# Kernel tuning notes

Measured on AMD Instinct MI355X. Metric: run time of the kernel, lower is better.

Reference implementation:

```python
import jax, jax.numpy as jnp
import numpy as np

B, IN_DIM, OUT_DIM = 16384, 1024, 512
N_CAPS, CAP_DIM = 8, 16


def squash(x, axis=-1):
    # scale = |x|^2 / (1 + |x|^2) ; out = scale * x / sqrt(|x|^2 + 1e-8)
    sq = jnp.sum(x * x, axis=axis, keepdims=True)
    return (sq / (1.0 + sq)) * x / jnp.sqrt(sq + 1e-8)


def setup_inputs() -> dict:
    key = jax.random.key(0)
    k1, k2, k3, k4 = jax.random.split(key, 4)
    x = jax.random.normal(k1, (B, IN_DIM), dtype=jnp.float32)
    # Linear(in_dim, n_caps*cap_dim) params (kaiming-ish scale)
    Wp = jax.random.normal(k2, (IN_DIM, N_CAPS * CAP_DIM), dtype=jnp.float32) / np.sqrt(IN_DIM)
    bp = jax.random.normal(k3, (N_CAPS * CAP_DIM,), dtype=jnp.float32) * 0.01
    # routing transform W: [n_caps, cap_dim, out_dim], init std 0.02 as in torch code
    W = jax.random.normal(k4, (N_CAPS, CAP_DIM, OUT_DIM), dtype=jnp.float32) * 0.02
    return {"x": x, "Wp": Wp, "bp": bp, "W": W, "n_routing": 3}


def reference(x, Wp, bp, W, n_routing):
    batch = x.shape[0]
    primary = x @ Wp + bp                                   # [B, n*d]
    primary = primary.reshape(batch, N_CAPS, CAP_DIM)       # [B, n, d]
    primary = squash(primary, axis=-1)
    u_hat = jnp.einsum('bnd,ndo->bno', primary, W)          # [B, n, o]
    b = jnp.zeros((batch, N_CAPS, 1), dtype=x.dtype)
    v = None
    for i in range(n_routing):
        c = jax.nn.softmax(b, axis=1)                       # [B, n, 1]
        s = jnp.sum(c * u_hat, axis=1)                      # [B, o]
        v = squash(s, axis=-1)                              # [B, o]
        if i < n_routing - 1:
            agreement = jnp.einsum('bno,bo->bn', u_hat, v)  # [B, n]
            b = b + agreement[..., None]
    return v
```

## Files before the change

kernel.cpp:

```cpp
#include <hip/hip_runtime.h>
#include <math.h>

typedef __attribute__((ext_vector_type(8))) short bf16x8;
typedef __attribute__((ext_vector_type(8))) unsigned short u16x8;
typedef __attribute__((ext_vector_type(4))) float f32x4;

__device__ __forceinline__ unsigned short f2bf(float f) {
  unsigned u = __float_as_uint(f);
  return (unsigned short)((u + 0x7FFFu + ((u >> 16) & 1u)) >> 16);
}
__device__ __forceinline__ float bf2f(unsigned short h) {
  return __uint_as_float(((unsigned)h) << 16);
}
__device__ __forceinline__ void cvt8(const float4& a, const float4& b,
                                     u16x8& h, u16x8& l) {
  float f[8] = {a.x, a.y, a.z, a.w, b.x, b.y, b.z, b.w};
#pragma unroll
  for (int i = 0; i < 8; ++i) {
    unsigned short hh = f2bf(f[i]);
    h[i] = hh;
    l[i] = f2bf(f[i] - bf2f(hh));
  }
}

__device__ const int PM36[36] = {0,0,0,0,0,0,0,0, 1,1,1,1,1,1,1, 2,2,2,2,2,2,
                                 3,3,3,3,3, 4,4,4,4, 5,5,5, 6,6, 7};
__device__ const int PN36[36] = {0,1,2,3,4,5,6,7, 1,2,3,4,5,6,7, 2,3,4,5,6,7,
                                 3,4,5,6,7, 4,5,6,7, 5,6,7, 6,7, 7};
__device__ __forceinline__ constexpr int gidx(int a, int b) {
  int m = a < b ? a : b, n = a < b ? b : a;
  return m * 8 - (m * (m - 1)) / 2 + (n - m);
}

__global__ __launch_bounds__(256) void caps_prep(
    const float* __restrict__ Wp, unsigned short* __restrict__ th,
    unsigned short* __restrict__ tl)
{
  __shared__ float tile[64][128];
  const int t = threadIdx.x, b = blockIdx.x;
  const float* src = Wp + (size_t)b * 64 * 128;
#pragma unroll
  for (int i = 0; i < 8; ++i) {
    int j = t + i * 256;
    int kk = j >> 5, q = j & 31;
    *(float4*)&tile[kk][q * 4] = *(const float4*)(src + kk * 128 + q * 4);
  }
  __syncthreads();
  const int col = t >> 1, kg0 = (t & 1) * 4;
  unsigned short hi[32], lo[32];
#pragma unroll
  for (int kk = 0; kk < 32; ++kk) {
    float v = tile[kg0 * 8 + kk][col];
    unsigned short h = f2bf(v);
    hi[kk] = h;
    lo[kk] = f2bf(v - bf2f(h));
  }
#pragma unroll
  for (int i = 0; i < 4; ++i) {
    size_t off = (size_t)b * 8192 + (size_t)(kg0 + i) * 1024 + (size_t)col * 8;
    u16x8 vh, vl;
#pragma unroll
    for (int e = 0; e < 8; ++e) { vh[e] = hi[i * 8 + e]; vl[e] = lo[i * 8 + e]; }
    *(u16x8*)(th + off) = vh;
    *(u16x8*)(tl + off) = vl;
  }
}

__global__ __launch_bounds__(256) void caps_prep2(
    const float* __restrict__ W, unsigned short* __restrict__ th,
    unsigned short* __restrict__ tl)
{
  int t = blockIdx.x * 256 + threadIdx.x;
#pragma unroll
  for (int h = 0; h < 2; ++h) {
    int c = t + h * 4096;
    int kt = c >> 12, rem = c & 4095;
    int kg = rem >> 9, col = rem & 511;
    int kbase = kt * 64 + kg * 8;
    u16x8 vh, vl;
#pragma unroll
    for (int e = 0; e < 8; ++e) {
      float v = W[(size_t)(kbase + e) * 512 + col];
      unsigned short hh = f2bf(v);
      vh[e] = hh;
      vl[e] = f2bf(v - bf2f(hh));
    }
    size_t off = ((size_t)(kt * 8 + kg) * 512 + col) * 8;
    *(u16x8*)(th + off) = vh;
    *(u16x8*)(tl + off) = vl;
  }
}

__global__ __launch_bounds__(256) void caps_gram(
    const float* __restrict__ W, float* __restrict__ M)
{
  int a = blockIdx.x * 16 + (threadIdx.x >> 4);
  int b = blockIdx.y * 16 + (threadIdx.x & 15);
  const float* wa = W + (size_t)a * 512;
  const float* wb = W + (size_t)b * 512;
  float acc = 0.f;
#pragma unroll 4
  for (int o = 0; o < 512; o += 4) {
    float4 x = *(const float4*)(wa + o);
    float4 y = *(const float4*)(wb + o);
    acc += x.x * y.x + x.y * y.y + x.z * y.z + x.w * y.w;
  }
  M[a * 128 + b] = acc;
}

#define LDSBUF 24576

__global__ __launch_bounds__(512) void caps_primary(
    const float* __restrict__ x, const unsigned short* __restrict__ bth,
    const unsigned short* __restrict__ btl, const float* __restrict__ bp,
    float* __restrict__ p_out)
{
  __shared__ unsigned short lds[2 * LDSBUF];
  const int tid  = threadIdx.x;
  const int lane = tid & 63;
  const int w    = tid >> 6;
  const int wm   = w >> 1;
  const int wn   = w & 1;
  const int row0 = blockIdx.x * 64;

  const int rowA = tid & 63;
  const int kgA  = tid >> 6;
  const float* xrow = x + (size_t)(row0 + rowA) * 1024;

  f32x4 acc[4];
#pragma unroll
  for (int j = 0; j < 4; ++j) acc[j] = (f32x4){0.f, 0.f, 0.f, 0.f};

  float4 a0, a1;
  u16x8 b0, b1, b2, b3;

#define STAGE_LOAD(kt) do { \
    const float* xp = xrow + (kt) * 64; \
    a0 = *(const float4*)(xp + kgA * 8); \
    a1 = *(const float4*)(xp + kgA * 8 + 4); \
    const unsigned short* bh_ = bth + (size_t)(kt) * 8192; \
    const unsigned short* bl_ = btl + (size_t)(kt) * 8192; \
    b0 = *(const u16x8*)(bh_ + (size_t)tid * 8); \
    b1 = *(const u16x8*)(bh_ + (size_t)(512 + tid) * 8); \
    b2 = *(const u16x8*)(bl_ + (size_t)tid * 8); \
    b3 = *(const u16x8*)(bl_ + (size_t)(512 + tid) * 8); \
  } while (0)

#define STAGE_WRITE(bufi) do { \
    u16x8 h0, l0; \
    cvt8(a0, a1, h0, l0); \
    unsigned short* B = lds + (bufi) * LDSBUF; \
    *(u16x8*)(B + kgA * 512 + rowA * 8) = h0; \
    *(u16x8*)(B + 4096 + kgA * 512 + rowA * 8) = l0; \
    *(u16x8*)(B + 8192  + tid * 8) = b0; \
    *(u16x8*)(B + 8192  + (512 + tid) * 8) = b1; \
    *(u16x8*)(B + 16384 + tid * 8) = b2; \
    *(u16x8*)(B + 16384 + (512 + tid) * 8) = b3; \
  } while (0)

#define COMPUTE(bufi) do { \
    const unsigned short* B = lds + (bufi) * LDSBUF; \
    _Pragma("unroll") \
    for (int s = 0; s < 2; ++s) { \
      const int kg = s * 4 + (lane >> 4); \
      const int rA = wm * 16 + (lane & 15); \
      const int cB = wn * 64 + (lane & 15); \
      bf16x8 ah = *(const bf16x8*)(B + kg * 512 + rA * 8); \
      bf16x8 al = *(const bf16x8*)(B + 4096 + kg * 512 + rA * 8); \
      _Pragma("unroll") \
      for (int nf = 0; nf < 4; ++nf) { \
        bf16x8 bh  = *(const bf16x8*)(B + 8192  + kg * 1024 + (cB + nf * 16) * 8); \
        bf16x8 blo = *(const bf16x8*)(B + 16384 + kg * 1024 + (cB + nf * 16) * 8); \
        acc[nf] = __builtin_amdgcn_mfma_f32_16x16x32_bf16(ah, bh,  acc[nf], 0, 0, 0); \
        acc[nf] = __builtin_amdgcn_mfma_f32_16x16x32_bf16(ah, blo, acc[nf], 0, 0, 0); \
        acc[nf] = __builtin_amdgcn_mfma_f32_16x16x32_bf16(al, bh,  acc[nf], 0, 0, 0); \
      } \
    } \
  } while (0)

  STAGE_LOAD(0);
  STAGE_WRITE(0);
  __syncthreads();
  for (int kt = 0; kt < 16; ++kt) {
    const int cur = kt & 1;
    if (kt < 15) STAGE_LOAD(kt + 1);
    COMPUTE(cur);
    if (kt < 15) STAGE_WRITE(cur ^ 1);
    __syncthreads();
  }

  const int ln = lane & 15, l4 = lane >> 4;
  float bpv[4];
#pragma unroll
  for (int nf = 0; nf < 4; ++nf) bpv[nf] = bp[wn * 64 + nf * 16 + ln];
#pragma unroll
  for (int nf = 0; nf < 4; ++nf)
#pragma unroll
    for (int r = 0; r < 4; ++r) {
      float val = acc[nf][r] + bpv[nf];
      float sq = val * val;
      sq += __shfl_xor(sq, 1); sq += __shfl_xor(sq, 2);
      sq += __shfl_xor(sq, 4); sq += __shfl_xor(sq, 8);
      float sc = (sq / (1.f + sq)) / sqrtf(sq + 1e-8f);
      p_out[(size_t)(row0 + wm * 16 + l4 * 4 + r) * 128 +
            wn * 64 + nf * 16 + ln] = val * sc;
    }
#undef STAGE_LOAD
#undef STAGE_WRITE
#undef COMPUTE
}

__global__ __launch_bounds__(256, 1) void caps_route_g(
    const float* __restrict__ p_in, const float* __restrict__ Mg,
    float* __restrict__ qout)
{
  __shared__ float p_lds[128 * 66];
  __shared__ float M_lds[16384];
  __shared__ float G_lds[64 * 37];
  __shared__ float cs_lds[64 * 9];
  const int tid  = threadIdx.x;
  const int lane = tid & 63;
  const int w    = tid >> 6;
  const int row0 = blockIdx.x * 64;

#pragma unroll
  for (int i = 0; i < 8; ++i) {
    int j = tid + i * 256;
    int r = j >> 5, c4 = j & 31;
    float4 v = *(const float4*)(p_in + (size_t)(row0 + r) * 128 + c4 * 4);
    p_lds[(c4 * 4 + 0) * 66 + r] = v.x;
    p_lds[(c4 * 4 + 1) * 66 + r] = v.y;
    p_lds[(c4 * 4 + 2) * 66 + r] = v.z;
    p_lds[(c4 * 4 + 3) * 66 + r] = v.w;
  }
#pragma unroll
  for (int i = 0; i < 16; ++i) {
    int j = tid + i * 256;
    *(float4*)&M_lds[j * 4] = *(const float4*)(Mg + j * 4);
  }
  __syncthreads();

  for (int i = 0; i < 9; ++i) {
    const int pi = w * 9 + i;
    const int m = PM36[pi], n = PN36[pi];
    float pm[16], pn[16];
#pragma unroll
    for (int j = 0; j < 16; ++j) pm[j] = p_lds[(m * 16 + j) * 66 + lane];
#pragma unroll
    for (int j = 0; j < 16; ++j) pn[j] = p_lds[(n * 16 + j) * 66 + lane];
    float acc = 0.f;
#pragma unroll
    for (int ii = 0; ii < 16; ++ii) {
      const float* Mr = &M_lds[(n * 16 + ii) * 128 + m * 16];
      float t = 0.f;
#pragma unroll
      for (int j4 = 0; j4 < 4; ++j4) {
        float4 mv = *(const float4*)(Mr + j4 * 4);
        t = fmaf(mv.x, pm[j4 * 4 + 0], t);
        t = fmaf(mv.y, pm[j4 * 4 + 1], t);
        t = fmaf(mv.z, pm[j4 * 4 + 2], t);
        t = fmaf(mv.w, pm[j4 * 4 + 3], t);
      }
      acc = fmaf(pn[ii], t, acc);
    }
    G_lds[lane * 37 + pi] = acc;
  }
  __syncthreads();

  if (w == 0) {
    float Gf[36];
#pragma unroll
    for (int j = 0; j < 36; ++j) Gf[j] = G_lds[lane * 37 + j];
    float bb[8] = {0.f, 0.f, 0.f, 0.f, 0.f, 0.f, 0.f, 0.f};
    float cs[8];
#pragma unroll
    for (int it = 0; it < 3; ++it) {
      float mx = bb[0];
#pragma unroll
      for (int n = 1; n < 8; ++n) mx = fmaxf(mx, bb[n]);
      float e[8], Z = 0.f;
#pragma unroll
      for (int n = 0; n < 8; ++n) { e[n] = expf(bb[n] - mx); Z += e[n]; }
      float inv = 1.f / Z;
      float c[8];
#pragma unroll
      for (int n = 0; n < 8; ++n) c[n] = e[n] * inv;
      float t[8] = {0.f, 0.f, 0.f, 0.f, 0.f, 0.f, 0.f, 0.f};
#pragma unroll
      for (int n = 0; n < 8; ++n)
#pragma unroll
        for (int m2 = 0; m2 < 8; ++m2)
          t[n] = fmaf(Gf[gidx(n, m2)], c[m2], t[n]);
      float ss = 0.f;
#pragma unroll
      for (int n = 0; n < 8; ++n) ss = fmaf(c[n], t[n], ss);
      float scale = (ss / (1.f + ss)) / sqrtf(ss + 1e-8f);
      if (it < 2) {
#pragma unroll
        for (int n = 0; n < 8; ++n) bb[n] += scale * t[n];
      } else {
#pragma unroll
        for (int n = 0; n < 8; ++n) cs[n] = scale * c[n];
      }
    }
#pragma unroll
    for (int n = 0; n < 8; ++n) cs_lds[lane * 9 + n] = cs[n];
  }
  __syncthreads();

#pragma unroll
  for (int i = 0; i < 8; ++i) {
    int j = tid + i * 256;
    int r = j >> 5, c4 = j & 31;
    float4 pv = *(const float4*)(p_in + (size_t)(row0 + r) * 128 + c4 * 4);
    float csv = cs_lds[r * 9 + (c4 >> 2)];
    *(float4*)(qout + (size_t)(row0 + r) * 128 + c4 * 4) =
        make_float4(pv.x * csv, pv.y * csv, pv.z * csv, pv.w * csv);
  }
}

__global__ __launch_bounds__(512) void caps_vout(
    const float* __restrict__ q, const unsigned short* __restrict__ bth,
    const unsigned short* __restrict__ btl, float* __restrict__ out)
{
  __shared__ unsigned short lds[LDSBUF];
  const int tid  = threadIdx.x;
  const int lane = tid & 63;
  const int w    = tid >> 6;
  const int wm   = w >> 1;
  const int wn   = w & 1;
  const int row0 = blockIdx.x * 64;
  const int col0 = blockIdx.y * 128;

  const int rowA = tid & 63;
  const int kgA  = tid >> 6;
  const float* qrow = q + (size_t)(row0 + rowA) * 128;

  f32x4 acc[4];
#pragma unroll
  for (int j = 0; j < 4; ++j) acc[j] = (f32x4){0.f, 0.f, 0.f, 0.f};

  float4 a0, a1;
  u16x8 b0, b1, b2, b3;

#define VSTAGE_LOAD(kt) do { \
    const float* xp = qrow + (kt) * 64; \
    a0 = *(const float4*)(xp + kgA * 8); \
    a1 = *(const float4*)(xp + kgA * 8 + 4); \
    const int kg0 = tid >> 7, col = tid & 127; \
    const size_t s0 = ((size_t)((kt) * 8 + kg0) * 512 + col0 + col) * 8; \
    const size_t s1 = ((size_t)((kt) * 8 + 4 + kg0) * 512 + col0 + col) * 8; \
    b0 = *(const u16x8*)(bth + s0); \
    b1 = *(const u16x8*)(bth + s1); \
    b2 = *(const u16x8*)(btl + s0); \
    b3 = *(const u16x8*)(btl + s1); \
  } while (0)

#define VSTAGE_WRITE() do { \
    u16x8 h0, l0; \
    cvt8(a0, a1, h0, l0); \
    *(u16x8*)(lds + kgA * 512 + rowA * 8) = h0; \
    *(u16x8*)(lds + 4096 + kgA * 512 + rowA * 8) = l0; \
    *(u16x8*)(lds + 8192  + tid * 8) = b0; \
    *(u16x8*)(lds + 12288 + tid * 8) = b1; \
    *(u16x8*)(lds + 16384 + tid * 8) = b2; \
    *(u16x8*)(lds + 20480 + tid * 8) = b3; \
  } while (0)

#define VCOMPUTE() do { \
    _Pragma("unroll") \
    for (int s = 0; s < 2; ++s) { \
      const int kg = s * 4 + (lane >> 4); \
      const int rA = wm * 16 + (lane & 15); \
      const int cB = wn * 64 + (lane & 15); \
      bf16x8 ah = *(const bf16x8*)(lds + kg * 512 + rA * 8); \
      bf16x8 al = *(const bf16x8*)(lds + 4096 + kg * 512 + rA * 8); \
      _Pragma("unroll") \
      for (int nf = 0; nf < 4; ++nf) { \
        bf16x8 bh  = *(const bf16x8*)(lds + 8192  + kg * 1024 + (cB + nf * 16) * 8); \
        bf16x8 blo = *(const bf16x8*)(lds + 16384 + kg * 1024 + (cB + nf * 16) * 8); \
        acc[nf] = __builtin_amdgcn_mfma_f32_16x16x32_bf16(ah, bh,  acc[nf], 0, 0, 0); \
        acc[nf] = __builtin_amdgcn_mfma_f32_16x16x32_bf16(ah, blo, acc[nf], 0, 0, 0); \
        acc[nf] = __builtin_amdgcn_mfma_f32_16x16x32_bf16(al, bh,  acc[nf], 0, 0, 0); \
      } \
    } \
  } while (0)

  VSTAGE_LOAD(0);
  VSTAGE_WRITE();
  __syncthreads();
  VSTAGE_LOAD(1);
  VCOMPUTE();
  __syncthreads();
  VSTAGE_WRITE();
  __syncthreads();
  VCOMPUTE();

  const int ln = lane & 15, l4 = lane >> 4;
#pragma unroll
  for (int nf = 0; nf < 4; ++nf)
#pragma unroll
    for (int r = 0; r < 4; ++r)
      out[(size_t)(row0 + wm * 16 + l4 * 4 + r) * 512 +
          col0 + wn * 64 + nf * 16 + ln] = acc[nf][r];
#undef VSTAGE_LOAD
#undef VSTAGE_WRITE
#undef VCOMPUTE
}

extern "C" void kernel_launch(void* const* d_in, const int* in_sizes, int n_in,
                              void* d_out, int out_size, void* d_ws, size_t ws_size,
                              hipStream_t stream) {
  (void)in_sizes; (void)n_in; (void)out_size; (void)ws_size;
  const float* x  = (const float*)d_in[0];
  const float* Wp = (const float*)d_in[1];
  const float* bp = (const float*)d_in[2];
  const float* W  = (const float*)d_in[3];
  char* ws = (char*)d_ws;
  float* p_ws = (float*)ws;
  unsigned short* th1 = (unsigned short*)(ws + 8388608);
  unsigned short* tl1 = (unsigned short*)(ws + 8650752);
  unsigned short* th2 = (unsigned short*)(ws + 8912896);
  unsigned short* tl2 = (unsigned short*)(ws + 9043968);
  float* Mws = (float*)(ws + 9175040);
  float* outp = (float*)d_out;

  caps_prep<<<16, 256, 0, stream>>>(Wp, th1, tl1);
  caps_prep2<<<16, 256, 0, stream>>>(W, th2, tl2);
  caps_gram<<<dim3(8, 8), 256, 0, stream>>>(W, Mws);
  caps_primary<<<256, 512, 0, stream>>>(x, th1, tl1, bp, p_ws);
  caps_route_g<<<256, 256, 0, stream>>>(p_ws, Mws, p_ws);
  caps_vout<<<dim3(256, 4), 512, 0, stream>>>(p_ws, th2, tl2, outp);
}
```

Before: 99.49 us.

## Merge prep kernels and drop LDS staging in primary GEMM

Folds the three weight-prep kernels (Wp split, W split, Gram matrix) into one launch with block-range dispatch, which removes two kernel launches. The primary projection GEMM no longer stages through LDS with double buffering: each wave reads x and the pre-split bf16 weights straight from global memory into MFMA operands, using 256-thread blocks over 32 rows and twice as many blocks. The output GEMM now loads its whole B slice into LDS once and reads A straight from global. This trades LDS traffic and barriers for more redundant global and L2 reads of the weights.

```diff
diff --git a/kernel.cpp b/kernel.cpp
--- a/kernel.cpp
+++ b/kernel.cpp
@@ -12,14 +12,14 @@
 __device__ __forceinline__ float bf2f(unsigned short h) {
   return __uint_as_float(((unsigned)h) << 16);
 }
-__device__ __forceinline__ void cvt8(const float4& a, const float4& b,
-                                     u16x8& h, u16x8& l) {
+__device__ __forceinline__ void cvt8b(const float4& a, const float4& b,
+                                      bf16x8& h, bf16x8& l) {
   float f[8] = {a.x, a.y, a.z, a.w, b.x, b.y, b.z, b.w};
 #pragma unroll
   for (int i = 0; i < 8; ++i) {
     unsigned short hh = f2bf(f[i]);
-    h[i] = hh;
-    l[i] = f2bf(f[i] - bf2f(hh));
+    h[i] = (short)hh;
+    l[i] = (short)f2bf(f[i] - bf2f(hh));
   }
 }
 
@@ -32,182 +32,137 @@
   return m * 8 - (m * (m - 1)) / 2 + (n - m);
 }
 
-__global__ __launch_bounds__(256) void caps_prep(
-    const float* __restrict__ Wp, unsigned short* __restrict__ th,
-    unsigned short* __restrict__ tl)
+__global__ __launch_bounds__(256) void caps_prep_all(
+    const float* __restrict__ Wp, const float* __restrict__ W,
+    unsigned short* __restrict__ th1, unsigned short* __restrict__ tl1,
+    unsigned short* __restrict__ th2, unsigned short* __restrict__ tl2,
+    float* __restrict__ M)
 {
   __shared__ float tile[64][128];
   const int t = threadIdx.x, b = blockIdx.x;
-  const float* src = Wp + (size_t)b * 64 * 128;
-#pragma unroll
-  for (int i = 0; i < 8; ++i) {
-    int j = t + i * 256;
-    int kk = j >> 5, q = j & 31;
-    *(float4*)&tile[kk][q * 4] = *(const float4*)(src + kk * 128 + q * 4);
-  }
-  __syncthreads();
-  const int col = t >> 1, kg0 = (t & 1) * 4;
-  unsigned short hi[32], lo[32];
-#pragma unroll
-  for (int kk = 0; kk < 32; ++kk) {
-    float v = tile[kg0 * 8 + kk][col];
-    unsigned short h = f2bf(v);
-    hi[kk] = h;
-    lo[kk] = f2bf(v - bf2f(h));
-  }
-#pragma unroll
-  for (int i = 0; i < 4; ++i) {
-    size_t off = (size_t)b * 8192 + (size_t)(kg0 + i) * 1024 + (size_t)col * 8;
-    u16x8 vh, vl;
-#pragma unroll
-    for (int e = 0; e < 8; ++e) { vh[e] = hi[i * 8 + e]; vl[e] = lo[i * 8 + e]; }
-    *(u16x8*)(th + off) = vh;
-    *(u16x8*)(tl + off) = vl;
-  }
-}
-
-__global__ __launch_bounds__(256) void caps_prep2(
-    const float* __restrict__ W, unsigned short* __restrict__ th,
-    unsigned short* __restrict__ tl)
-{
-  int t = blockIdx.x * 256 + threadIdx.x;
-#pragma unroll
-  for (int h = 0; h < 2; ++h) {
-    int c = t + h * 4096;
-    int kt = c >> 12, rem = c & 4095;
-    int kg = rem >> 9, col = rem & 511;
-    int kbase = kt * 64 + kg * 8;
-    u16x8 vh, vl;
-#pragma unroll
-    for (int e = 0; e < 8; ++e) {
-      float v = W[(size_t)(kbase + e) * 512 + col];
-      unsigned short hh = f2bf(v);
-      vh[e] = hh;
-      vl[e] = f2bf(v - bf2f(hh));
-    }
-    size_t off = ((size_t)(kt * 8 + kg) * 512 + col) * 8;
-    *(u16x8*)(th + off) = vh;
-    *(u16x8*)(tl + off) = vl;
-  }
-}
-
-__global__ __launch_bounds__(256) void caps_gram(
-    const float* __restrict__ W, float* __restrict__ M)
-{
-  int a = blockIdx.x * 16 + (threadIdx.x >> 4);
-  int b = blockIdx.y * 16 + (threadIdx.x & 15);
-  const float* wa = W + (size_t)a * 512;
-  const float* wb = W + (size_t)b * 512;
-  float acc = 0.f;
+  if (b < 16) {
+    const float* src = Wp + (size_t)b * 64 * 128;
+#pragma unroll
+    for (int i = 0; i < 8; ++i) {
+      int j = t + i * 256;
+      int kk = j >> 5, q = j & 31;
+      *(float4*)&tile[kk][q * 4] = *(const float4*)(src + kk * 128 + q * 4);
+    }
+    __syncthreads();
+    const int col = t >> 1, kg0 = (t & 1) * 4;
+    unsigned short hi[32], lo[32];
+#pragma unroll
+    for (int kk = 0; kk < 32; ++kk) {
+      float v = tile[kg0 * 8 + kk][col];
+      unsigned short h = f2bf(v);
+      hi[kk] = h;
+      lo[kk] = f2bf(v - bf2f(h));
+    }
+#pragma unroll
+    for (int i = 0; i < 4; ++i) {
+      size_t off = (size_t)b * 8192 + (size_t)(kg0 + i) * 1024 + (size_t)col * 8;
+      u16x8 vh, vl;
+#pragma unroll
+      for (int e = 0; e < 8; ++e) { vh[e] = hi[i * 8 + e]; vl[e] = lo[i * 8 + e]; }
+      *(u16x8*)(th1 + off) = vh;
+      *(u16x8*)(tl1 + off) = vl;
+    }
+  } else if (b < 32) {
+    int tt = (b - 16) * 256 + t;
+#pragma unroll
+    for (int h = 0; h < 2; ++h) {
+      int c = tt + h * 4096;
+      int kt = c >> 12, rem = c & 4095;
+      int kg = rem >> 9, col = rem & 511;
+      int kbase = kt * 64 + kg * 8;
+      u16x8 vh, vl;
+#pragma unroll
+      for (int e = 0; e < 8; ++e) {
+        float v = W[(size_t)(kbase + e) * 512 + col];
+        unsigned short hh = f2bf(v);
+        vh[e] = hh;
+        vl[e] = f2bf(v - bf2f(hh));
+      }
+      size_t off = ((size_t)(kt * 8 + kg) * 512 + col) * 8;
+      *(u16x8*)(th2 + off) = vh;
+      *(u16x8*)(tl2 + off) = vl;
+    }
+  } else {
+    int bb = b - 32;
+    int a = (bb >> 3) * 16 + (t >> 4);
+    int c = (bb & 7) * 16 + (t & 15);
+    const float* wa = W + (size_t)a * 512;
+    const float* wb = W + (size_t)c * 512;
+    float acc = 0.f;
 #pragma unroll 4
-  for (int o = 0; o < 512; o += 4) {
-    float4 x = *(const float4*)(wa + o);
-    float4 y = *(const float4*)(wb + o);
-    acc += x.x * y.x + x.y * y.y + x.z * y.z + x.w * y.w;
-  }
-  M[a * 128 + b] = acc;
-}
-
-#define LDSBUF 24576
-
-__global__ __launch_bounds__(512) void caps_primary(
+    for (int o = 0; o < 512; o += 4) {
+      float4 xx = *(const float4*)(wa + o);
+      float4 yy = *(const float4*)(wb + o);
+      acc += xx.x * yy.x + xx.y * yy.y + xx.z * yy.z + xx.w * yy.w;
+    }
+    M[a * 128 + c] = acc;
+  }
+}
+
+__global__ __launch_bounds__(256) void caps_primary(
     const float* __restrict__ x, const unsigned short* __restrict__ bth,
     const unsigned short* __restrict__ btl, const float* __restrict__ bp,
     float* __restrict__ p_out)
 {
-  __shared__ unsigned short lds[2 * LDSBUF];
-  const int tid  = threadIdx.x;
-  const int lane = tid & 63;
-  const int w    = tid >> 6;
-  const int wm   = w >> 1;
-  const int wn   = w & 1;
-  const int row0 = blockIdx.x * 64;
-
-  const int rowA = tid & 63;
-  const int kgA  = tid >> 6;
-  const float* xrow = x + (size_t)(row0 + rowA) * 1024;
+  const int tid = threadIdx.x, lane = tid & 63, w = tid >> 6;
+  const int rowg = w >> 1, ch = w & 1;
+  const int cb = lane & 15, kgl = lane >> 4;
+  const int rA = blockIdx.x * 32 + rowg * 16 + cb;
+  const float* xp = x + (size_t)rA * 1024;
+  const bf16x8* Bh = (const bf16x8*)bth;
+  const bf16x8* Bl = (const bf16x8*)btl;
+  const int bb0 = kgl * 128 + ch * 64 + cb;
 
   f32x4 acc[4];
 #pragma unroll
   for (int j = 0; j < 4; ++j) acc[j] = (f32x4){0.f, 0.f, 0.f, 0.f};
 
-  float4 a0, a1;
-  u16x8 b0, b1, b2, b3;
-
-#define STAGE_LOAD(kt) do { \
-    const float* xp = xrow + (kt) * 64; \
-    a0 = *(const float4*)(xp + kgA * 8); \
-    a1 = *(const float4*)(xp + kgA * 8 + 4); \
-    const unsigned short* bh_ = bth + (size_t)(kt) * 8192; \
-    const unsigned short* bl_ = btl + (size_t)(kt) * 8192; \
-    b0 = *(const u16x8*)(bh_ + (size_t)tid * 8); \
-    b1 = *(const u16x8*)(bh_ + (size_t)(512 + tid) * 8); \
-    b2 = *(const u16x8*)(bl_ + (size_t)tid * 8); \
-    b3 = *(const u16x8*)(bl_ + (size_t)(512 + tid) * 8); \
-  } while (0)
-
-#define STAGE_WRITE(bufi) do { \
-    u16x8 h0, l0; \
-    cvt8(a0, a1, h0, l0); \
-    unsigned short* B = lds + (bufi) * LDSBUF; \
-    *(u16x8*)(B + kgA * 512 + rowA * 8) = h0; \
-    *(u16x8*)(B + 4096 + kgA * 512 + rowA * 8) = l0; \
-    *(u16x8*)(B + 8192  + tid * 8) = b0; \
-    *(u16x8*)(B + 8192  + (512 + tid) * 8) = b1; \
-    *(u16x8*)(B + 16384 + tid * 8) = b2; \
-    *(u16x8*)(B + 16384 + (512 + tid) * 8) = b3; \
-  } while (0)
-
-#define COMPUTE(bufi) do { \
-    const unsigned short* B = lds + (bufi) * LDSBUF; \
-    _Pragma("unroll") \
-    for (int s = 0; s < 2; ++s) { \
-      const int kg = s * 4 + (lane >> 4); \
-      const int rA = wm * 16 + (lane & 15); \
-      const int cB = wn * 64 + (lane & 15); \
-      bf16x8 ah = *(const bf16x8*)(B + kg * 512 + rA * 8); \
-      bf16x8 al = *(const bf16x8*)(B + 4096 + kg * 512 + rA * 8); \
-      _Pragma("unroll") \
-      for (int nf = 0; nf < 4; ++nf) { \
-        bf16x8 bh  = *(const bf16x8*)(B + 8192  + kg * 1024 + (cB + nf * 16) * 8); \
-        bf16x8 blo = *(const bf16x8*)(B + 16384 + kg * 1024 + (cB + nf * 16) * 8); \
-        acc[nf] = __builtin_amdgcn_mfma_f32_16x16x32_bf16(ah, bh,  acc[nf], 0, 0, 0); \
-        acc[nf] = __builtin_amdgcn_mfma_f32_16x16x32_bf16(ah, blo, acc[nf], 0, 0, 0); \
-        acc[nf] = __builtin_amdgcn_mfma_f32_16x16x32_bf16(al, bh,  acc[nf], 0, 0, 0); \
-      } \
-    } \
-  } while (0)
-
-  STAGE_LOAD(0);
-  STAGE_WRITE(0);
-  __syncthreads();
+#pragma unroll 2
   for (int kt = 0; kt < 16; ++kt) {
-    const int cur = kt & 1;
-    if (kt < 15) STAGE_LOAD(kt + 1);
-    COMPUTE(cur);
-    if (kt < 15) STAGE_WRITE(cur ^ 1);
-    __syncthreads();
-  }
-
-  const int ln = lane & 15, l4 = lane >> 4;
-  float bpv[4];
-#pragma unroll
-  for (int nf = 0; nf < 4; ++nf) bpv[nf] = bp[wn * 64 + nf * 16 + ln];
-#pragma unroll
-  for (int nf = 0; nf < 4; ++nf)
+    const float* xk = xp + kt * 64 + kgl * 8;
+    float4 a00 = *(const float4*)(xk);
+    float4 a01 = *(const float4*)(xk + 4);
+    float4 a10 = *(const float4*)(xk + 32);
+    float4 a11 = *(const float4*)(xk + 36);
+    bf16x8 ah0, al0, ah1, al1;
+    cvt8b(a00, a01, ah0, al0);
+    cvt8b(a10, a11, ah1, al1);
+    const int kb = bb0 + kt * 1024;
+#pragma unroll
+    for (int nf = 0; nf < 4; ++nf) {
+      bf16x8 bh0 = Bh[kb + nf * 16];
+      bf16x8 bl0 = Bl[kb + nf * 16];
+      bf16x8 bh1 = Bh[kb + 512 + nf * 16];
+      bf16x8 bl1 = Bl[kb + 512 + nf * 16];
+      acc[nf] = __builtin_amdgcn_mfma_f32_16x16x32_bf16(ah0, bh0, acc[nf], 0, 0, 0);
+      acc[nf] = __builtin_amdgcn_mfma_f32_16x16x32_bf16(ah0, bl0, acc[nf], 0, 0, 0);
+      acc[nf] = __builtin_amdgcn_mfma_f32_16x16x32_bf16(al0, bh0, acc[nf], 0, 0, 0);
+      acc[nf] = __builtin_amdgcn_mfma_f32_16x16x32_bf16(ah1, bh1, acc[nf], 0, 0, 0);
+      acc[nf] = __builtin_amdgcn_mfma_f32_16x16x32_bf16(ah1, bl1, acc[nf], 0, 0, 0);
+      acc[nf] = __builtin_amdgcn_mfma_f32_16x16x32_bf16(al1, bh1, acc[nf], 0, 0, 0);
+    }
+  }
+
+  const int l4 = lane >> 4;
+#pragma unroll
+  for (int nf = 0; nf < 4; ++nf) {
+    float bpv = bp[ch * 64 + nf * 16 + cb];
 #pragma unroll
     for (int r = 0; r < 4; ++r) {
-      float val = acc[nf][r] + bpv[nf];
+      float val = acc[nf][r] + bpv;
       float sq = val * val;
       sq += __shfl_xor(sq, 1); sq += __shfl_xor(sq, 2);
       sq += __shfl_xor(sq, 4); sq += __shfl_xor(sq, 8);
       float sc = (sq / (1.f + sq)) / sqrtf(sq + 1e-8f);
-      p_out[(size_t)(row0 + wm * 16 + l4 * 4 + r) * 128 +
-            wn * 64 + nf * 16 + ln] = val * sc;
-    }
-#undef STAGE_LOAD
-#undef STAGE_WRITE
-#undef COMPUTE
+      p_out[(size_t)(blockIdx.x * 32 + rowg * 16 + l4 * 4 + r) * 128 +
+            ch * 64 + nf * 16 + cb] = val * sc;
+    }
+  }
 }
 
 __global__ __launch_bounds__(256, 1) void caps_route_g(
@@ -323,7 +278,7 @@
     const float* __restrict__ q, const unsigned short* __restrict__ bth,
     const unsigned short* __restrict__ btl, float* __restrict__ out)
 {
-  __shared__ unsigned short lds[LDSBUF];
+  __shared__ unsigned short Bsh[32768];
   const int tid  = threadIdx.x;
   const int lane = tid & 63;
   const int w    = tid >> 6;
@@ -332,80 +287,59 @@
   const int row0 = blockIdx.x * 64;
   const int col0 = blockIdx.y * 128;
 
-  const int rowA = tid & 63;
-  const int kgA  = tid >> 6;
-  const float* qrow = q + (size_t)(row0 + rowA) * 128;
+#pragma unroll
+  for (int i = 0; i < 4; ++i) {
+    int idx = tid + i * 512;
+    int kt = idx >> 10, kg = (idx >> 7) & 7, col = idx & 127;
+    size_t g = ((size_t)(kt * 8 + kg) * 512 + col0 + col) * 8;
+    *(u16x8*)&Bsh[idx * 8] = *(const u16x8*)(bth + g);
+    *(u16x8*)&Bsh[16384 + idx * 8] = *(const u16x8*)(btl + g);
+  }
+  __syncthreads();
+
+  const int cb = lane & 15, kgl = lane >> 4;
+  const int rA = row0 + wm * 16 + cb;
+  const float* qp = q + (size_t)rA * 128;
 
   f32x4 acc[4];
 #pragma unroll
   for (int j = 0; j < 4; ++j) acc[j] = (f32x4){0.f, 0.f, 0.f, 0.f};
 
-  float4 a0, a1;
-  u16x8 b0, b1, b2, b3;
-
-#define VSTAGE_LOAD(kt) do { \
-    const float* xp = qrow + (kt) * 64; \
-    a0 = *(const float4*)(xp + kgA * 8); \
-    a1 = *(const float4*)(xp + kgA * 8 + 4); \
-    const int kg0 = tid >> 7, col = tid & 127; \
-    const size_t s0 = ((size_t)((kt) * 8 + kg0) * 512 + col0 + col) * 8; \
-    const size_t s1 = ((size_t)((kt) * 8 + 4 + kg0) * 512 + col0 + col) * 8; \
-    b0 = *(const u16x8*)(bth + s0); \
-    b1 = *(const u16x8*)(bth + s1); \
-    b2 = *(const u16x8*)(btl + s0); \
-    b3 = *(const u16x8*)(btl + s1); \
-  } while (0)
-
-#define VSTAGE_WRITE() do { \
-    u16x8 h0, l0; \
-    cvt8(a0, a1, h0, l0); \
-    *(u16x8*)(lds + kgA * 512 + rowA * 8) = h0; \
-    *(u16x8*)(lds + 4096 + kgA * 512 + rowA * 8) = l0; \
-    *(u16x8*)(lds + 8192  + tid * 8) = b0; \
-    *(u16x8*)(lds + 12288 + tid * 8) = b1; \
-    *(u16x8*)(lds + 16384 + tid * 8) = b2; \
-    *(u16x8*)(lds + 20480 + tid * 8) = b3; \
-  } while (0)
-
-#define VCOMPUTE() do { \
-    _Pragma("unroll") \
-    for (int s = 0; s < 2; ++s) { \
-      const int kg = s * 4 + (lane >> 4); \
-      const int rA = wm * 16 + (lane & 15); \
-      const int cB = wn * 64 + (lane & 15); \
-      bf16x8 ah = *(const bf16x8*)(lds + kg * 512 + rA * 8); \
-      bf16x8 al = *(const bf16x8*)(lds + 4096 + kg * 512 + rA * 8); \
-      _Pragma("unroll") \
-      for (int nf = 0; nf < 4; ++nf) { \
-        bf16x8 bh  = *(const bf16x8*)(lds + 8192  + kg * 1024 + (cB + nf * 16) * 8); \
-        bf16x8 blo = *(const bf16x8*)(lds + 16384 + kg * 1024 + (cB + nf * 16) * 8); \
-        acc[nf] = __builtin_amdgcn_mfma_f32_16x16x32_bf16(ah, bh,  acc[nf], 0, 0, 0); \
-        acc[nf] = __builtin_amdgcn_mfma_f32_16x16x32_bf16(ah, blo, acc[nf], 0, 0, 0); \
-        acc[nf] = __builtin_amdgcn_mfma_f32_16x16x32_bf16(al, bh,  acc[nf], 0, 0, 0); \
-      } \
-    } \
-  } while (0)
-
-  VSTAGE_LOAD(0);
-  VSTAGE_WRITE();
-  __syncthreads();
-  VSTAGE_LOAD(1);
-  VCOMPUTE();
-  __syncthreads();
-  VSTAGE_WRITE();
-  __syncthreads();
-  VCOMPUTE();
-
-  const int ln = lane & 15, l4 = lane >> 4;
+#pragma unroll
+  for (int kt = 0; kt < 2; ++kt) {
+    const float* qk = qp + kt * 64 + kgl * 8;
+    float4 a00 = *(const float4*)(qk);
+    float4 a01 = *(const float4*)(qk + 4);
+    float4 a10 = *(const float4*)(qk + 32);
+    float4 a11 = *(const float4*)(qk + 36);
+    bf16x8 ah0, al0, ah1, al1;
+    cvt8b(a00, a01, ah0, al0);
+    cvt8b(a10, a11, ah1, al1);
+#pragma unroll
+    for (int nf = 0; nf < 4; ++nf) {
+      int c = wn * 64 + nf * 16 + cb;
+      int i0 = ((kt * 8 + kgl) * 128 + c) * 8;
+      int i1 = ((kt * 8 + 4 + kgl) * 128 + c) * 8;
+      bf16x8 bh0 = *(const bf16x8*)&Bsh[i0];
+      bf16x8 bl0 = *(const bf16x8*)&Bsh[16384 + i0];
+      bf16x8 bh1 = *(const bf16x8*)&Bsh[i1];
+      bf16x8 bl1 = *(const bf16x8*)&Bsh[16384 + i1];
+      acc[nf] = __builtin_amdgcn_mfma_f32_16x16x32_bf16(ah0, bh0, acc[nf], 0, 0, 0);
+      acc[nf] = __builtin_amdgcn_mfma_f32_16x16x32_bf16(ah0, bl0, acc[nf], 0, 0, 0);
+      acc[nf] = __builtin_amdgcn_mfma_f32_16x16x32_bf16(al0, bh0, acc[nf], 0, 0, 0);
+      acc[nf] = __builtin_amdgcn_mfma_f32_16x16x32_bf16(ah1, bh1, acc[nf], 0, 0, 0);
+      acc[nf] = __builtin_amdgcn_mfma_f32_16x16x32_bf16(ah1, bl1, acc[nf], 0, 0, 0);
+      acc[nf] = __builtin_amdgcn_mfma_f32_16x16x32_bf16(al1, bh1, acc[nf], 0, 0, 0);
+    }
+  }
+
+  const int l4 = lane >> 4;
 #pragma unroll
   for (int nf = 0; nf < 4; ++nf)
 #pragma unroll
     for (int r = 0; r < 4; ++r)
       out[(size_t)(row0 + wm * 16 + l4 * 4 + r) * 512 +
-          col0 + wn * 64 + nf * 16 + ln] = acc[nf][r];
-#undef VSTAGE_LOAD
-#undef VSTAGE_WRITE
-#undef VCOMPUTE
+          col0 + wn * 64 + nf * 16 + cb] = acc[nf][r];
 }
 
 extern "C" void kernel_launch(void* const* d_in, const int* in_sizes, int n_in,
@@ -425,10 +359,8 @@
   float* Mws = (float*)(ws + 9175040);
   float* outp = (float*)d_out;
 
-  caps_prep<<<16, 256, 0, stream>>>(Wp, th1, tl1);
-  caps_prep2<<<16, 256, 0, stream>>>(W, th2, tl2);
-  caps_gram<<<dim3(8, 8), 256, 0, stream>>>(W, Mws);
-  caps_primary<<<256, 512, 0, stream>>>(x, th1, tl1, bp, p_ws);
+  caps_prep_all<<<96, 256, 0, stream>>>(Wp, W, th1, tl1, th2, tl2, Mws);
+  caps_primary<<<512, 256, 0, stream>>>(x, th1, tl1, bp, p_ws);
   caps_route_g<<<256, 256, 0, stream>>>(p_ws, Mws, p_ws);
   caps_vout<<<dim3(256, 4), 512, 0, stream>>>(p_ws, th2, tl2, outp);
 }
```

Measured after the change: 120.1 us. 20.7% more time.
